# Kernel tuning notes

Measured on AMD Instinct MI355X. Metric: run time of the kernel, lower is better.

## Reference

```python
import jax, jax.numpy as jnp
import numpy as np

N = 50000      # nodes
E = 800000     # directed edges (before self-loops)
IN = 128       # in_channels
H = 4          # heads (layers 1,2)
C = 64         # hidden_channels per head
OUT = 512      # out_channels of final Linear
LEAKY_SLOPE = 0.2


def _gat_layer(x, src, dst, n, W, a_src, a_dst, b, concat):
    """PyG GATConv (v1): shared linear, additive attention, segment softmax over dst."""
    heads, ch = a_src.shape
    xl = (x @ W).reshape(n, heads, ch)                       # [N,H,C]
    as_n = jnp.sum(xl * a_src, axis=-1)                      # [N,H] alpha_src per node
    ad_n = jnp.sum(xl * a_dst, axis=-1)                      # [N,H] alpha_dst per node
    logits = jax.nn.leaky_relu(as_n[src] + ad_n[dst], LEAKY_SLOPE)  # [Etot,H]
    m = jax.lax.stop_gradient(jax.ops.segment_max(logits, dst, num_segments=n))
    p = jnp.exp(logits - m[dst])
    denom = jax.ops.segment_sum(p, dst, num_segments=n) + 1e-16
    alpha = p / denom[dst]                                   # segment softmax over incoming edges
    out = jax.ops.segment_sum(xl[src] * alpha[:, :, None], dst, num_segments=n)  # [N,H,C]
    out = out.reshape(n, heads * ch) if concat else out.mean(axis=1)
    return out + b


def setup_inputs() -> dict:
    key = jax.random.key(0)
    ks = jax.random.split(key, 16)

    def gl(k, shape, fan_in):
        return jax.random.normal(k, shape, dtype=jnp.float32) * np.float32(1.0 / np.sqrt(fan_in))

    x = jax.random.normal(ks[0], (N, IN), dtype=jnp.float32)
    edge_index = jax.random.randint(ks[1], (2, E), 0, N, dtype=jnp.int32)

    inp = {
        "x": x,
        "edge_index": edge_index,
        # layer 1: in -> H*C (concat)
        "W1": gl(ks[2], (IN, H * C), IN),
        "a_src1": gl(ks[3], (H, C), C),
        "a_dst1": gl(ks[4], (H, C), C),
        "b1": jnp.zeros((H * C,), jnp.float32),
        # layer 2: H*C -> H*C (concat)
        "W2": gl(ks[5], (H * C, H * C), H * C),
        "a_src2": gl(ks[6], (H, C), C),
        "a_dst2": gl(ks[7], (H, C), C),
        "b2": jnp.zeros((H * C,), jnp.float32),
        # layer 3: H*C -> C (1 head, no concat)
        "W3": gl(ks[8], (H * C, C), H * C),
        "a_src3": gl(ks[9], (1, C), C),
        "a_dst3": gl(ks[10], (1, C), C),
        "b3": jnp.zeros((C,), jnp.float32),
        # final fc: C -> OUT
        "Wfc": gl(ks[11], (C, OUT), C),
        "bfc": jnp.zeros((OUT,), jnp.float32),
    }
    return inp


def reference(x, edge_index, W1, a_src1, a_dst1, b1, W2, a_src2, a_dst2, b2,
              W3, a_src3, a_dst3, b3, Wfc, bfc):
    n = x.shape[0]
    loop = jnp.arange(n, dtype=edge_index.dtype)             # PyG GATConv adds self-loops
    src = jnp.concatenate([edge_index[0], loop])
    dst = jnp.concatenate([edge_index[1], loop])

    h = jax.nn.relu(_gat_layer(x, src, dst, n, W1, a_src1, a_dst1, b1, True))
    h = jax.nn.relu(_gat_layer(h, src, dst, n, W2, a_src2, a_dst2, b2, True))
    h = jax.nn.relu(_gat_layer(h, src, dst, n, W3, a_src3, a_dst3, b3, False))
    return jax.nn.relu(h @ Wfc + bfc)                        # [N, OUT]
```

## Files before the change

kernel.cpp:

```cpp
#include <hip/hip_runtime.h>
#include <cstdint>
#include <cstddef>

typedef unsigned short ushort_t;
typedef __bf16 bf16x8 __attribute__((ext_vector_type(8)));
typedef float f32x4 __attribute__((ext_vector_type(4)));

__device__ __forceinline__ float b2f(ushort_t u) {
    return __uint_as_float(((unsigned int)u) << 16);
}
__device__ __forceinline__ ushort_t f2b(float f) {
    __bf16 h = (__bf16)f;
    return *(ushort_t*)&h;
}

__device__ __forceinline__ void stage8(const float* __restrict__ g, ushort_t* s) {
    float4 f0 = *(const float4*)g;
    float4 f1 = *(const float4*)(g + 4);
    union { ushort_t u[8]; uint4 v; } t;
    t.u[0] = f2b(f0.x); t.u[1] = f2b(f0.y); t.u[2] = f2b(f0.z); t.u[3] = f2b(f0.w);
    t.u[4] = f2b(f1.x); t.u[5] = f2b(f1.y); t.u[6] = f2b(f1.z); t.u[7] = f2b(f1.w);
    *(uint4*)s = t.v;
}
__device__ __forceinline__ void stage8(const ushort_t* __restrict__ g, ushort_t* s) {
    *(float4*)s = *(const float4*)g;
}

__global__ __launch_bounds__(256) void transpose_kernel(const float* __restrict__ W,
                                                        ushort_t* __restrict__ WT,
                                                        int K, int N2) {
    int id = blockIdx.x * 256 + threadIdx.x;
    if (id >= K * N2) return;
    int n = id / K, k = id - n * K;
    WT[id] = f2b(W[k * N2 + n]);
}

__global__ __launch_bounds__(256) void degree_kernel(const int* __restrict__ ei_dst,
                                                     int* __restrict__ deg, int E, int Etot) {
    int e = blockIdx.x * 256 + threadIdx.x;
    if (e >= Etot) return;
    int d = (e < E) ? ei_dst[e] : (e - E);
    atomicAdd(&deg[d], 1);
}

__global__ __launch_bounds__(256) void partial_sum_kernel(const int* __restrict__ deg,
                                                          int* __restrict__ bsum, int n) {
    __shared__ int ws[4];
    int t = threadIdx.x;
    int i = blockIdx.x * 256 + t;
    int v = (i < n) ? deg[i] : 0;
#pragma unroll
    for (int off = 32; off; off >>= 1) v += __shfl_xor(v, off, 64);
    if ((t & 63) == 0) ws[t >> 6] = v;
    __syncthreads();
    if (t == 0) bsum[blockIdx.x] = ws[0] + ws[1] + ws[2] + ws[3];
}

__global__ __launch_bounds__(256) void scan_bsum_kernel(const int* __restrict__ bsum,
                                                        int* __restrict__ boff,
                                                        int* __restrict__ rowoff,
                                                        int nblk, int n) {
    __shared__ int sm[256];
    int t = threadIdx.x;
    int v = (t < nblk) ? bsum[t] : 0;
    sm[t] = v;
    __syncthreads();
#pragma unroll
    for (int off = 1; off < 256; off <<= 1) {
        int u = (t >= off) ? sm[t - off] : 0;
        __syncthreads();
        sm[t] += u;
        __syncthreads();
    }
    if (t < nblk) boff[t] = sm[t] - v;
    if (t == 255) rowoff[n] = sm[255];
}

__global__ __launch_bounds__(256) void block_scan_kernel(const int* __restrict__ deg,
                                                         const int* __restrict__ boff,
                                                         int* __restrict__ rowoff, int n) {
    __shared__ int sm[256];
    int t = threadIdx.x;
    int i = blockIdx.x * 256 + t;
    int v = (i < n) ? deg[i] : 0;
    sm[t] = v;
    __syncthreads();
#pragma unroll
    for (int off = 1; off < 256; off <<= 1) {
        int u = (t >= off) ? sm[t - off] : 0;
        __syncthreads();
        sm[t] += u;
        __syncthreads();
    }
    if (i < n) rowoff[i] = boff[blockIdx.x] + sm[t] - v;
}

__global__ __launch_bounds__(256) void scatter_kernel(const int* __restrict__ ei_src,
                                                      const int* __restrict__ ei_dst,
                                                      const int* __restrict__ rowoff,
                                                      int* __restrict__ cursor,
                                                      int* __restrict__ ssrc, int E, int Etot) {
    int e = blockIdx.x * 256 + threadIdx.x;
    if (e >= Etot) return;
    int s, d;
    if (e < E) { s = ei_src[e]; d = ei_dst[e]; } else { s = d = e - E; }
    int pos = rowoff[d] + atomicAdd(&cursor[d], 1);
    ssrc[pos] = s;
}

template <typename TA, bool EPI>
__global__ __launch_bounds__(256) void gemm_mfma(const TA* __restrict__ A,
                                                 const ushort_t* __restrict__ WT,
                                                 float* __restrict__ C,
                                                 ushort_t* __restrict__ Cb,
                                                 const float* __restrict__ bias,
                                                 int M, int K, int N2) {
    __shared__ ushort_t sA[64 * 32];
    __shared__ ushort_t sB[64 * 32];
    const int tid = threadIdx.x;
    const int wv = tid >> 6, lane = tid & 63;
    const int quad = lane >> 4, l16 = lane & 15;
    const int bm = blockIdx.x * 64, bn = blockIdx.y * 64;
    const int srow = tid >> 2, skof = (tid & 3) * 8;
    f32x4 acc[4] = {};

    for (int k0 = 0; k0 < K; k0 += 32) {
        int gm = bm + srow;
        gm = gm < M ? gm : M - 1;
        stage8(A + (size_t)gm * K + k0 + skof, sA + srow * 32 + skof);
        stage8(WT + (size_t)(bn + srow) * K + k0 + skof, sB + srow * 32 + skof);
        __syncthreads();

        bf16x8 af = *(const bf16x8*)(sA + (wv * 16 + l16) * 32 + quad * 8);
#pragma unroll
        for (int j = 0; j < 4; j++) {
            bf16x8 bf = *(const bf16x8*)(sB + (j * 16 + l16) * 32 + quad * 8);
            acc[j] = __builtin_amdgcn_mfma_f32_16x16x32_bf16(af, bf, acc[j], 0, 0, 0);
        }
        __syncthreads();
    }

#pragma unroll
    for (int j = 0; j < 4; j++) {
        int col = bn + j * 16 + l16;
        float bv = EPI ? bias[col] : 0.f;
#pragma unroll
        for (int r = 0; r < 4; r++) {
            int row = bm + wv * 16 + quad * 4 + r;
            if (row < M) {
                float v = acc[j][r];
                if (EPI) {
                    v += bv;
                    v = v > 0.f ? v : 0.f;
                    C[(size_t)row * N2 + col] = v;
                } else {
                    Cb[(size_t)row * N2 + col] = f2b(v);
                }
            }
        }
    }
}

template <int CH>
__global__ __launch_bounds__(256) void attn_kernel(const ushort_t* __restrict__ xl,
                                                   const float* __restrict__ a_src,
                                                   const float* __restrict__ a_dst,
                                                   float* __restrict__ as_n,
                                                   float* __restrict__ ad_n, int N) {
    int n = blockIdx.x * 4 + (threadIdx.x >> 6);
    int lane = threadIdx.x & 63;
    if (n >= N) return;
    if (CH == 256) {
        ushort4 u = ((const ushort4*)xl)[(size_t)n * 64 + lane];
        float4 av = ((const float4*)a_src)[lane];
        float4 dv = ((const float4*)a_dst)[lane];
        float x0 = b2f(u.x), x1 = b2f(u.y), x2 = b2f(u.z), x3 = b2f(u.w);
        float s = x0 * av.x + x1 * av.y + x2 * av.z + x3 * av.w;
        float d = x0 * dv.x + x1 * dv.y + x2 * dv.z + x3 * dv.w;
#pragma unroll
        for (int off = 8; off; off >>= 1) {
            s += __shfl_xor(s, off, 64);
            d += __shfl_xor(d, off, 64);
        }
        if ((lane & 15) == 0) {
            int h = lane >> 4;
            as_n[n * 4 + h] = s;
            ad_n[n * 4 + h] = d;
        }
    } else {
        float xv = b2f(xl[(size_t)n * 64 + lane]);
        float s = xv * a_src[lane];
        float d = xv * a_dst[lane];
#pragma unroll
        for (int off = 32; off; off >>= 1) {
            s += __shfl_xor(s, off, 64);
            d += __shfl_xor(d, off, 64);
        }
        if (lane == 0) { as_n[n] = s; ad_n[n] = d; }
    }
}

template <int CH>
__global__ __launch_bounds__(256) void aggregate_kernel(const ushort_t* __restrict__ xl,
                                                        const float* __restrict__ as_n,
                                                        const float* __restrict__ ad_n,
                                                        const int* __restrict__ rowoff,
                                                        const int* __restrict__ ssrc,
                                                        const float* __restrict__ bias,
                                                        ushort_t* __restrict__ hout, int N) {
    int dd = blockIdx.x * 4 + (threadIdx.x >> 6);
    int lane = threadIdx.x & 63;
    if (dd >= N) return;
    int r0 = rowoff[dd], r1 = rowoff[dd + 1];
    if (CH == 256) {
        const int h = lane >> 4;
        const float adv = ad_n[dd * 4 + h];
        const ushort4* xv = (const ushort4*)xl;
        float a0 = 0.f, a1 = 0.f, a2 = 0.f, a3 = 0.f, den = 0.f;
        int i = r0;
        for (; i + 4 <= r1; i += 4) {
            int s0 = ssrc[i], s1 = ssrc[i + 1], s2 = ssrc[i + 2], s3 = ssrc[i + 3];
            float g0 = as_n[s0 * 4 + h], g1 = as_n[s1 * 4 + h];
            float g2 = as_n[s2 * 4 + h], g3 = as_n[s3 * 4 + h];
            ushort4 u0 = xv[(size_t)s0 * 64 + lane];
            ushort4 u1 = xv[(size_t)s1 * 64 + lane];
            ushort4 u2 = xv[(size_t)s2 * 64 + lane];
            ushort4 u3 = xv[(size_t)s3 * 64 + lane];
            float l0 = g0 + adv; l0 = l0 > 0.f ? l0 : 0.2f * l0;
            float l1 = g1 + adv; l1 = l1 > 0.f ? l1 : 0.2f * l1;
            float l2 = g2 + adv; l2 = l2 > 0.f ? l2 : 0.2f * l2;
            float l3 = g3 + adv; l3 = l3 > 0.f ? l3 : 0.2f * l3;
            float p0 = __expf(l0), p1 = __expf(l1), p2 = __expf(l2), p3 = __expf(l3);
            den += p0 + p1 + p2 + p3;
            a0 += p0 * b2f(u0.x) + p1 * b2f(u1.x) + p2 * b2f(u2.x) + p3 * b2f(u3.x);
            a1 += p0 * b2f(u0.y) + p1 * b2f(u1.y) + p2 * b2f(u2.y) + p3 * b2f(u3.y);
            a2 += p0 * b2f(u0.z) + p1 * b2f(u1.z) + p2 * b2f(u2.z) + p3 * b2f(u3.z);
            a3 += p0 * b2f(u0.w) + p1 * b2f(u1.w) + p2 * b2f(u2.w) + p3 * b2f(u3.w);
        }
        for (; i < r1; i++) {
            int s = ssrc[i];
            float lg = as_n[s * 4 + h] + adv;
            lg = lg > 0.f ? lg : 0.2f * lg;
            float p = __expf(lg);
            den += p;
            ushort4 u = xv[(size_t)s * 64 + lane];
            a0 += p * b2f(u.x);
            a1 += p * b2f(u.y);
            a2 += p * b2f(u.z);
            a3 += p * b2f(u.w);
        }
        float di = 1.f / (den + 1e-16f);
        float4 bv = ((const float4*)bias)[lane];
        float v0 = a0 * di + bv.x;
        float v1 = a1 * di + bv.y;
        float v2 = a2 * di + bv.z;
        float v3 = a3 * di + bv.w;
        ushort4 o;
        o.x = f2b(v0 > 0.f ? v0 : 0.f);
        o.y = f2b(v1 > 0.f ? v1 : 0.f);
        o.z = f2b(v2 > 0.f ? v2 : 0.f);
        o.w = f2b(v3 > 0.f ? v3 : 0.f);
        ((ushort4*)hout)[(size_t)dd * 64 + lane] = o;
    } else {
        const float adv = ad_n[dd];
        float a0 = 0.f, den = 0.f;
        int i = r0;
        for (; i + 4 <= r1; i += 4) {
            int s0 = ssrc[i], s1 = ssrc[i + 1], s2 = ssrc[i + 2], s3 = ssrc[i + 3];
            float g0 = as_n[s0], g1 = as_n[s1], g2 = as_n[s2], g3 = as_n[s3];
            ushort_t u0 = xl[(size_t)s0 * 64 + lane];
            ushort_t u1 = xl[(size_t)s1 * 64 + lane];
            ushort_t u2 = xl[(size_t)s2 * 64 + lane];
            ushort_t u3 = xl[(size_t)s3 * 64 + lane];
            float l0 = g0 + adv; l0 = l0 > 0.f ? l0 : 0.2f * l0;
            float l1 = g1 + adv; l1 = l1 > 0.f ? l1 : 0.2f * l1;
            float l2 = g2 + adv; l2 = l2 > 0.f ? l2 : 0.2f * l2;
            float l3 = g3 + adv; l3 = l3 > 0.f ? l3 : 0.2f * l3;
            float p0 = __expf(l0), p1 = __expf(l1), p2 = __expf(l2), p3 = __expf(l3);
            den += p0 + p1 + p2 + p3;
            a0 += p0 * b2f(u0) + p1 * b2f(u1) + p2 * b2f(u2) + p3 * b2f(u3);
        }
        for (; i < r1; i++) {
            int s = ssrc[i];
            float lg = as_n[s] + adv;
            lg = lg > 0.f ? lg : 0.2f * lg;
            float p = __expf(lg);
            den += p;
            a0 += p * b2f(xl[(size_t)s * 64 + lane]);
        }
        float v = a0 / (den + 1e-16f) + bias[lane];
        hout[(size_t)dd * 64 + lane] = f2b(v > 0.f ? v : 0.f);
    }
}

extern "C" void kernel_launch(void* const* d_in, const int* in_sizes, int n_in,
                              void* d_out, int out_size, void* d_ws, size_t ws_size,
                              hipStream_t stream) {
    const int N = in_sizes[0] / 128;
    const int E = in_sizes[1] / 2;
    const int Etot = E + N;

    const float* x = (const float*)d_in[0];
    const int* ei = (const int*)d_in[1];
    const int* ei_src = ei;
    const int* ei_dst = ei + E;
    float* out = (float*)d_out;

    const float* as1 = (const float*)d_in[3];
    const float* ad1 = (const float*)d_in[4];
    const float* b1  = (const float*)d_in[5];
    const float* as2 = (const float*)d_in[7];
    const float* ad2 = (const float*)d_in[8];
    const float* b2  = (const float*)d_in[9];
    const float* as3 = (const float*)d_in[11];
    const float* ad3 = (const float*)d_in[12];
    const float* b3  = (const float*)d_in[13];
    const float* bfc = (const float*)d_in[15];

    ushort_t* bufX = (ushort_t*)d_ws;
    ushort_t* bufH = bufX + (size_t)N * 256;
    ushort_t* W1T  = bufH + (size_t)N * 256;
    ushort_t* W2T  = W1T + 32768;
    ushort_t* W3T  = W2T + 65536;
    ushort_t* WfcT = W3T + 16384;
    float* asn = (float*)(WfcT + 32768);
    float* adn = asn + (size_t)N * 4;
    int* deg    = (int*)(adn + (size_t)N * 4);
    int* rowoff = deg + N;
    int* cursor = rowoff + N + 1;
    int* ssrc   = cursor + N;
    int* bsum   = ssrc + Etot;
    int* boff   = bsum + 256;

    transpose_kernel<<<(128 * 256 + 255) / 256, 256, 0, stream>>>((const float*)d_in[2], W1T, 128, 256);
    transpose_kernel<<<(256 * 256 + 255) / 256, 256, 0, stream>>>((const float*)d_in[6], W2T, 256, 256);
    transpose_kernel<<<(256 * 64 + 255) / 256, 256, 0, stream>>>((const float*)d_in[10], W3T, 256, 64);
    transpose_kernel<<<(64 * 512 + 255) / 256, 256, 0, stream>>>((const float*)d_in[14], WfcT, 64, 512);

    hipMemsetAsync(deg, 0, (size_t)(3 * N + 1) * sizeof(int), stream);
    int eb = (Etot + 255) / 256;
    degree_kernel<<<eb, 256, 0, stream>>>(ei_dst, deg, E, Etot);
    const int NBLK = (N + 255) / 256;
    partial_sum_kernel<<<NBLK, 256, 0, stream>>>(deg, bsum, N);
    scan_bsum_kernel<<<1, 256, 0, stream>>>(bsum, boff, rowoff, NBLK, N);
    block_scan_kernel<<<NBLK, 256, 0, stream>>>(deg, boff, rowoff, N);
    scatter_kernel<<<eb, 256, 0, stream>>>(ei_src, ei_dst, rowoff, cursor, ssrc, E, Etot);

    const int MB = (N + 63) / 64;
    int nb4 = (N + 3) / 4;

    gemm_mfma<float, false><<<dim3(MB, 4), 256, 0, stream>>>(x, W1T, nullptr, bufX, nullptr, N, 128, 256);
    attn_kernel<256><<<nb4, 256, 0, stream>>>(bufX, as1, ad1, asn, adn, N);
    aggregate_kernel<256><<<nb4, 256, 0, stream>>>(bufX, asn, adn, rowoff, ssrc, b1, bufH, N);

    gemm_mfma<ushort_t, false><<<dim3(MB, 4), 256, 0, stream>>>(bufH, W2T, nullptr, bufX, nullptr, N, 256, 256);
    attn_kernel<256><<<nb4, 256, 0, stream>>>(bufX, as2, ad2, asn, adn, N);
    aggregate_kernel<256><<<nb4, 256, 0, stream>>>(bufX, asn, adn, rowoff, ssrc, b2, bufH, N);

    gemm_mfma<ushort_t, false><<<dim3(MB, 1), 256, 0, stream>>>(bufH, W3T, nullptr, bufX, nullptr, N, 256, 64);
    attn_kernel<64><<<nb4, 256, 0, stream>>>(bufX, as3, ad3, asn, adn, N);
    aggregate_kernel<64><<<nb4, 256, 0, stream>>>(bufX, asn, adn, rowoff, ssrc, b3, bufH, N);

    gemm_mfma<ushort_t, true><<<dim3(MB, 8), 256, 0, stream>>>(bufH, WfcT, out, nullptr, bfc, N, 64, 512);
}
```

Baseline: 511.1 us.

## Precompute per-edge attention weights in separate kernel; widen aggregate gather to 8 edges

Adds an edge_p_kernel that computes exp(leaky_relu(as[src]+ad[dst])) once per edge and head into a buffer, with scatter now also writing sorted dst indices. The aggregate kernel then reads precomputed weights instead of gathering as_n and recomputing exp in every lane, and its loop now batches 8 edges with a masked tail so more independent gathers are in flight. The cost is an extra kernel launch per layer plus writing and reading an Etot*4 float buffer and a second index array.

New measurement: 528.8 us. 1.03x slower.

```diff
diff --git a/kernel.cpp b/kernel.cpp
--- a/kernel.cpp
+++ b/kernel.cpp
@@ -99,13 +99,38 @@
                                                       const int* __restrict__ ei_dst,
                                                       const int* __restrict__ rowoff,
                                                       int* __restrict__ cursor,
-                                                      int* __restrict__ ssrc, int E, int Etot) {
+                                                      int* __restrict__ ssrc,
+                                                      int* __restrict__ sdst, int E, int Etot) {
     int e = blockIdx.x * 256 + threadIdx.x;
     if (e >= Etot) return;
     int s, d;
     if (e < E) { s = ei_src[e]; d = ei_dst[e]; } else { s = d = e - E; }
     int pos = rowoff[d] + atomicAdd(&cursor[d], 1);
     ssrc[pos] = s;
+    sdst[pos] = d;
+}
+
+template <int H>
+__global__ __launch_bounds__(256) void edge_p_kernel(const int* __restrict__ ssrc,
+                                                     const int* __restrict__ sdst,
+                                                     const float* __restrict__ as_n,
+                                                     const float* __restrict__ ad_n,
+                                                     float* __restrict__ p, int Etot) {
+    int id = blockIdx.x * 256 + threadIdx.x;
+    if (H == 4) {
+        if (id >= Etot * 4) return;
+        int e = id >> 2, h = id & 3;
+        int s = ssrc[e], d = sdst[e];
+        float lg = as_n[s * 4 + h] + ad_n[d * 4 + h];
+        lg = lg > 0.f ? lg : 0.2f * lg;
+        p[id] = __expf(lg);
+    } else {
+        if (id >= Etot) return;
+        int s = ssrc[id], d = sdst[id];
+        float lg = as_n[s] + ad_n[d];
+        lg = lg > 0.f ? lg : 0.2f * lg;
+        p[id] = __expf(lg);
+    }
 }
 
 template <typename TA, bool EPI>
@@ -202,8 +227,7 @@
 
 template <int CH>
 __global__ __launch_bounds__(256) void aggregate_kernel(const ushort_t* __restrict__ xl,
-                                                        const float* __restrict__ as_n,
-                                                        const float* __restrict__ ad_n,
+                                                        const float* __restrict__ pp,
                                                         const int* __restrict__ rowoff,
                                                         const int* __restrict__ ssrc,
                                                         const float* __restrict__ bias,
@@ -214,40 +238,30 @@
     int r0 = rowoff[dd], r1 = rowoff[dd + 1];
     if (CH == 256) {
         const int h = lane >> 4;
-        const float adv = ad_n[dd * 4 + h];
         const ushort4* xv = (const ushort4*)xl;
         float a0 = 0.f, a1 = 0.f, a2 = 0.f, a3 = 0.f, den = 0.f;
-        int i = r0;
-        for (; i + 4 <= r1; i += 4) {
-            int s0 = ssrc[i], s1 = ssrc[i + 1], s2 = ssrc[i + 2], s3 = ssrc[i + 3];
-            float g0 = as_n[s0 * 4 + h], g1 = as_n[s1 * 4 + h];
-            float g2 = as_n[s2 * 4 + h], g3 = as_n[s3 * 4 + h];
-            ushort4 u0 = xv[(size_t)s0 * 64 + lane];
-            ushort4 u1 = xv[(size_t)s1 * 64 + lane];
-            ushort4 u2 = xv[(size_t)s2 * 64 + lane];
-            ushort4 u3 = xv[(size_t)s3 * 64 + lane];
-            float l0 = g0 + adv; l0 = l0 > 0.f ? l0 : 0.2f * l0;
-            float l1 = g1 + adv; l1 = l1 > 0.f ? l1 : 0.2f * l1;
-            float l2 = g2 + adv; l2 = l2 > 0.f ? l2 : 0.2f * l2;
-            float l3 = g3 + adv; l3 = l3 > 0.f ? l3 : 0.2f * l3;
-            float p0 = __expf(l0), p1 = __expf(l1), p2 = __expf(l2), p3 = __expf(l3);
-            den += p0 + p1 + p2 + p3;
-            a0 += p0 * b2f(u0.x) + p1 * b2f(u1.x) + p2 * b2f(u2.x) + p3 * b2f(u3.x);
-            a1 += p0 * b2f(u0.y) + p1 * b2f(u1.y) + p2 * b2f(u2.y) + p3 * b2f(u3.y);
-            a2 += p0 * b2f(u0.z) + p1 * b2f(u1.z) + p2 * b2f(u2.z) + p3 * b2f(u3.z);
-            a3 += p0 * b2f(u0.w) + p1 * b2f(u1.w) + p2 * b2f(u2.w) + p3 * b2f(u3.w);
-        }
-        for (; i < r1; i++) {
-            int s = ssrc[i];
-            float lg = as_n[s * 4 + h] + adv;
-            lg = lg > 0.f ? lg : 0.2f * lg;
-            float p = __expf(lg);
-            den += p;
-            ushort4 u = xv[(size_t)s * 64 + lane];
-            a0 += p * b2f(u.x);
-            a1 += p * b2f(u.y);
-            a2 += p * b2f(u.z);
-            a3 += p * b2f(u.w);
+        for (int i = r0; i < r1; i += 8) {
+            int idx[8];
+            float pv[8];
+            ushort4 u[8];
+#pragma unroll
+            for (int j = 0; j < 8; j++) {
+                int t = i + j;
+                int id2 = t < r1 ? t : r0;
+                idx[j] = ssrc[id2];
+                float pw = pp[id2 * 4 + h];
+                pv[j] = t < r1 ? pw : 0.f;
+            }
+#pragma unroll
+            for (int j = 0; j < 8; j++) u[j] = xv[(size_t)idx[j] * 64 + lane];
+#pragma unroll
+            for (int j = 0; j < 8; j++) {
+                den += pv[j];
+                a0 += pv[j] * b2f(u[j].x);
+                a1 += pv[j] * b2f(u[j].y);
+                a2 += pv[j] * b2f(u[j].z);
+                a3 += pv[j] * b2f(u[j].w);
+            }
         }
         float di = 1.f / (den + 1e-16f);
         float4 bv = ((const float4*)bias)[lane];
@@ -262,31 +276,26 @@
         o.w = f2b(v3 > 0.f ? v3 : 0.f);
         ((ushort4*)hout)[(size_t)dd * 64 + lane] = o;
     } else {
-        const float adv = ad_n[dd];
         float a0 = 0.f, den = 0.f;
-        int i = r0;
-        for (; i + 4 <= r1; i += 4) {
-            int s0 = ssrc[i], s1 = ssrc[i + 1], s2 = ssrc[i + 2], s3 = ssrc[i + 3];
-            float g0 = as_n[s0], g1 = as_n[s1], g2 = as_n[s2], g3 = as_n[s3];
-            ushort_t u0 = xl[(size_t)s0 * 64 + lane];
-            ushort_t u1 = xl[(size_t)s1 * 64 + lane];
-            ushort_t u2 = xl[(size_t)s2 * 64 + lane];
-            ushort_t u3 = xl[(size_t)s3 * 64 + lane];
-            float l0 = g0 + adv; l0 = l0 > 0.f ? l0 : 0.2f * l0;
-            float l1 = g1 + adv; l1 = l1 > 0.f ? l1 : 0.2f * l1;
-            float l2 = g2 + adv; l2 = l2 > 0.f ? l2 : 0.2f * l2;
-            float l3 = g3 + adv; l3 = l3 > 0.f ? l3 : 0.2f * l3;
-            float p0 = __expf(l0), p1 = __expf(l1), p2 = __expf(l2), p3 = __expf(l3);
-            den += p0 + p1 + p2 + p3;
-            a0 += p0 * b2f(u0) + p1 * b2f(u1) + p2 * b2f(u2) + p3 * b2f(u3);
-        }
-        for (; i < r1; i++) {
-            int s = ssrc[i];
-            float lg = as_n[s] + adv;
-            lg = lg > 0.f ? lg : 0.2f * lg;
-            float p = __expf(lg);
-            den += p;
-            a0 += p * b2f(xl[(size_t)s * 64 + lane]);
+        for (int i = r0; i < r1; i += 8) {
+            int idx[8];
+            float pv[8];
+            ushort_t u[8];
+#pragma unroll
+            for (int j = 0; j < 8; j++) {
+                int t = i + j;
+                int id2 = t < r1 ? t : r0;
+                idx[j] = ssrc[id2];
+                float pw = pp[id2];
+                pv[j] = t < r1 ? pw : 0.f;
+            }
+#pragma unroll
+            for (int j = 0; j < 8; j++) u[j] = xl[(size_t)idx[j] * 64 + lane];
+#pragma unroll
+            for (int j = 0; j < 8; j++) {
+                den += pv[j];
+                a0 += pv[j] * b2f(u[j]);
+            }
         }
         float v = a0 / (den + 1e-16f) + bias[lane];
         hout[(size_t)dd * 64 + lane] = f2b(v > 0.f ? v : 0.f);
@@ -329,8 +338,10 @@
     int* rowoff = deg + N;
     int* cursor = rowoff + N + 1;
     int* ssrc   = cursor + N;
-    int* bsum   = ssrc + Etot;
+    int* sdst   = ssrc + Etot;
+    int* bsum   = sdst + Etot;
     int* boff   = bsum + 256;
+    float* pbuf = (float*)(boff + 256);
 
     transpose_kernel<<<(128 * 256 + 255) / 256, 256, 0, stream>>>((const float*)d_in[2], W1T, 128, 256);
     transpose_kernel<<<(256 * 256 + 255) / 256, 256, 0, stream>>>((const float*)d_in[6], W2T, 256, 256);
@@ -344,22 +355,27 @@
     partial_sum_kernel<<<NBLK, 256, 0, stream>>>(deg, bsum, N);
     scan_bsum_kernel<<<1, 256, 0, stream>>>(bsum, boff, rowoff, NBLK, N);
     block_scan_kernel<<<NBLK, 256, 0, stream>>>(deg, boff, rowoff, N);
-    scatter_kernel<<<eb, 256, 0, stream>>>(ei_src, ei_dst, rowoff, cursor, ssrc, E, Etot);
+    scatter_kernel<<<eb, 256, 0, stream>>>(ei_src, ei_dst, rowoff, cursor, ssrc, sdst, E, Etot);
 
     const int MB = (N + 63) / 64;
     int nb4 = (N + 3) / 4;
+    int epb4 = (Etot * 4 + 255) / 256;
+    int epb1 = (Etot + 255) / 256;
 
     gemm_mfma<float, false><<<dim3(MB, 4), 256, 0, stream>>>(x, W1T, nullptr, bufX, nullptr, N, 128, 256);
     attn_kernel<256><<<nb4, 256, 0, stream>>>(bufX, as1, ad1, asn, adn, N);
-    aggregate_kernel<256><<<nb4, 256, 0, stream>>>(bufX, asn, adn, rowoff, ssrc, b1, bufH, N);
+    edge_p_kernel<4><<<epb4, 256, 0, stream>>>(ssrc, sdst, asn, adn, pbuf, Etot);
+    aggregate_kernel<256><<<nb4, 256, 0, stream>>>(bufX, pbuf, rowoff, ssrc, b1, bufH, N);
 
     gemm_mfma<ushort_t, false><<<dim3(MB, 4), 256, 0, stream>>>(bufH, W2T, nullptr, bufX, nullptr, N, 256, 256);
     attn_kernel<256><<<nb4, 256, 0, stream>>>(bufX, as2, ad2, asn, adn, N);
-    aggregate_kernel<256><<<nb4, 256, 0, stream>>>(bufX, asn, adn, rowoff, ssrc, b2, bufH, N);
+    edge_p_kernel<4><<<epb4, 256, 0, stream>>>(ssrc, sdst, asn, adn, pbuf, Etot);
+    aggregate_kernel<256><<<nb4, 256, 0, stream>>>(bufX, pbuf, rowoff, ssrc, b2, bufH, N);
 
     gemm_mfma<ushort_t, false><<<dim3(MB, 1), 256, 0, stream>>>(bufH, W3T, nullptr, bufX, nullptr, N, 256, 64);
     attn_kernel<64><<<nb4, 256, 0, stream>>>(bufX, as3, ad3, asn, adn, N);
-    aggregate_kernel<64><<<nb4, 256, 0, stream>>>(bufX, asn, adn, rowoff, ssrc, b3, bufH, N);
+    edge_p_kernel<1><<<epb1, 256, 0, stream>>>(ssrc, sdst, asn, adn, pbuf, Etot);
+    aggregate_kernel<64><<<nb4, 256, 0, stream>>>(bufX, pbuf, rowoff, ssrc, b3, bufH, N);
 
     gemm_mfma<ushort_t, true><<<dim3(MB, 8), 256, 0, stream>>>(bufH, WfcT, out, nullptr, bfc, N, 64, 512);
 }
```
